# Kernel optimization log

Measured on AMD Instinct MI355X. Metric: run time of the kernel, lower is better.

The kernel has to match this reference:

```python
import jax, jax.numpy as jnp
import numpy as np

V, D, H, L, RATIO, T_MAX = 1024, 512, 8, 11, 3, 1024
DH = D // H
HID = D * RATIO
NB, DB = 2048, 128  # bigram buckets / dim
EPS = 1e-6


def _rope_tables(T):
    pos = jnp.arange(T, dtype=jnp.float32)
    freqs = 1.0 / (10000.0 ** (jnp.arange(0, DH, 2, dtype=jnp.float32) / DH))
    emb = jnp.outer(pos, freqs)  # [T, DH/2]
    return jnp.cos(emb), jnp.sin(emb)


def _rmsnorm(x, w):
    return x * jax.lax.rsqrt(jnp.mean(x * x, axis=-1, keepdims=True) + EPS) * w


def setup_inputs() -> dict:
    key = jax.random.key(0)
    ks = jax.random.split(key, 10)
    B, T = 8, 1024
    s = 0.02
    return {
        "x": jax.random.randint(ks[0], (B, T), 0, V),
        "embed": jax.random.normal(ks[1], (V, D), jnp.float32) * s,
        "Wqkv": jax.random.normal(ks[2], (L, 3 * D, D), jnp.float32) * s,
        "Wproj": jax.random.normal(ks[3], (L, D, D), jnp.float32) * s,
        "n1_w": jnp.ones((L, D), jnp.float32),
        "n2_w": jnp.ones((L, D), jnp.float32),
        "Wfc1": jax.random.normal(ks[4], (L, HID, D), jnp.float32) * s,
        "Wfc2": jax.random.normal(ks[5], (L, D, HID), jnp.float32) * s,
        "norm_f_w": jnp.ones((D,), jnp.float32),
        "bg_embed": jax.random.normal(ks[6], (NB, DB), jnp.float32) * s,
        "bg_proj": jax.random.normal(ks[7], (V, DB), jnp.float32) * s,
    }


def _attn(x, Wqkv, Wproj, cos, sin, causal):
    B, T, C = x.shape
    qkv = x @ Wqkv.T  # [B,T,3D]
    q, k, v = jnp.split(qkv, 3, axis=-1)
    def heads(t):
        return t.reshape(B, T, H, DH).transpose(0, 2, 1, 3)  # [B,H,T,DH]
    q, k, v = heads(q), heads(k), heads(v)
    c = cos[None, None]  # [1,1,T,DH/2]
    s = sin[None, None]
    def rope(t):
        t1, t2 = t[..., : DH // 2], t[..., DH // 2 :]
        return jnp.concatenate([t1 * c - t2 * s, t1 * s + t2 * c], axis=-1)
    q, k = rope(q), rope(k)
    w = jnp.einsum("bhqd,bhkd->bhqk", q, k) * (DH ** -0.5)
    w = jnp.where(causal, w, -jnp.inf)
    w = jax.nn.softmax(w.astype(jnp.float32), axis=-1).astype(x.dtype)
    out = jnp.einsum("bhqk,bhkd->bhqd", w, v)
    self_w = jnp.diagonal(w, axis1=-2, axis2=-1)[..., None]  # [B,H,T,1]
    out = out - self_w * v  # XSA: subtract self-value contribution
    out = out.transpose(0, 2, 1, 3).reshape(B, T, C)
    return out @ Wproj.T


def reference(x, embed, Wqkv, Wproj, n1_w, n2_w, Wfc1, Wfc2, norm_f_w, bg_embed, bg_proj):
    B, T = x.shape
    cos, sin = _rope_tables(T_MAX)
    cos, sin = cos[:T], sin[:T]
    causal = jnp.tril(jnp.ones((T, T), dtype=bool))
    # bigram logits from previous token
    prev = jnp.concatenate([jnp.zeros((B, 1), x.dtype), x[:, :-1]], axis=1)
    bigram_logits = bg_embed[prev % NB] @ bg_proj.T  # [B,T,V]
    h = embed[x]
    for i in range(L):
        h = h + _attn(_rmsnorm(h, n1_w[i]), Wqkv[i], Wproj[i], cos, sin, causal)
        z = _rmsnorm(h, n2_w[i])
        h = h + jnp.square(jax.nn.relu(z @ Wfc1[i].T)) @ Wfc2[i].T
    h = _rmsnorm(h, norm_f_w)
    return h @ embed.T + bigram_logits
```

## Files before the change

kernel.cpp:

```cpp
#include <hip/hip_runtime.h>

#define NROW   8192
#define DMODEL 512
#define TSEQ   1024
#define LAYERS 11
#define HIDDEN 1536

typedef __bf16 bf16_t;
typedef bf16_t bf16x8 __attribute__((ext_vector_type(8)));
typedef bf16_t bf16x4 __attribute__((ext_vector_type(4)));
typedef float  f32x4  __attribute__((ext_vector_type(4)));
typedef unsigned int u32;
typedef u32 u32x4 __attribute__((ext_vector_type(4)));

#define GLD16(gp, lp) __builtin_amdgcn_global_load_lds( \
    (const __attribute__((address_space(1))) void*)(gp), \
    (__attribute__((address_space(3))) void*)(lp), 16, 0, 0)

#if __has_builtin(__builtin_amdgcn_exp2f)
#define EXP2(x) __builtin_amdgcn_exp2f(x)
#else
#define EXP2(x) exp2f(x)
#endif

__global__ void rope_table_k(float* __restrict__ cosT, float* __restrict__ sinT) {
    int i = blockIdx.x * blockDim.x + threadIdx.x;
    int t = i >> 5, j = i & 31;
    float freq = powf(10000.f, -(float)j * (1.f / 32.f));
    float ang = (float)t * freq;
    cosT[i] = cosf(ang);
    sinT[i] = sinf(ang);
}

__global__ void embed_gather_k(const int* __restrict__ x,
                               const float* __restrict__ embed,
                               float* __restrict__ h,
                               bf16_t* __restrict__ hb) {
    int n = blockIdx.x;
    int d = threadIdx.x;
    float4 v = ((const float4*)(embed + (size_t)x[n] * DMODEL))[d];
    ((float4*)(h + (size_t)n * DMODEL))[d] = v;
    bf16x4 o;
    o[0] = (bf16_t)v.x; o[1] = (bf16_t)v.y; o[2] = (bf16_t)v.z; o[3] = (bf16_t)v.w;
    *(bf16x4*)(hb + (size_t)n * DMODEL + d * 4) = o;
}

__global__ void bg_gather_k(const int* __restrict__ x,
                            const float* __restrict__ bge,
                            bf16_t* __restrict__ Afu) {
    int n = blockIdx.x;
    int t = n & (TSEQ - 1);
    int prev = (t == 0) ? 0 : x[n - 1];
    Afu[(size_t)n * 640 + 512 + threadIdx.x] = (bf16_t)bge[(size_t)prev * 128 + threadIdx.x];
}

__global__ void cvt_bf16_k(const float* __restrict__ in, bf16_t* __restrict__ out, int n8) {
    int i = blockIdx.x * blockDim.x + threadIdx.x;
    if (i >= n8) return;
    float4 a = ((const float4*)in)[2 * i];
    float4 b = ((const float4*)in)[2 * i + 1];
    bf16x8 o;
    o[0] = (bf16_t)a.x; o[1] = (bf16_t)a.y; o[2] = (bf16_t)a.z; o[3] = (bf16_t)a.w;
    o[4] = (bf16_t)b.x; o[5] = (bf16_t)b.y; o[6] = (bf16_t)b.z; o[7] = (bf16_t)b.w;
    ((bf16x8*)out)[i] = o;
}

__global__ void cvt_fold_k(const float* __restrict__ in,
                           const float* __restrict__ nw,
                           bf16_t* __restrict__ out, int n8, int layerSz) {
    int i = blockIdx.x * blockDim.x + threadIdx.x;
    if (i >= n8) return;
    int i8 = i * 8;
    int k = i8 & 511;
    int l = i8 / layerSz;
    const float* wv = nw + l * DMODEL + k;
    float4 a = ((const float4*)in)[2 * i];
    float4 b = ((const float4*)in)[2 * i + 1];
    float4 wa = *(const float4*)wv;
    float4 wb = *(const float4*)(wv + 4);
    bf16x8 o;
    o[0] = (bf16_t)(a.x * wa.x); o[1] = (bf16_t)(a.y * wa.y);
    o[2] = (bf16_t)(a.z * wa.z); o[3] = (bf16_t)(a.w * wa.w);
    o[4] = (bf16_t)(b.x * wb.x); o[5] = (bf16_t)(b.y * wb.y);
    o[6] = (bf16_t)(b.z * wb.z); o[7] = (bf16_t)(b.w * wb.w);
    ((bf16x8*)out)[i] = o;
}

__global__ void cvt_pad_k(const float* __restrict__ in, bf16_t* __restrict__ out,
                          int n8, int lshift, int mask, int colOff) {
    int i = blockIdx.x * blockDim.x + threadIdx.x;
    if (i >= n8) return;
    int i8 = i * 8;
    int row = i8 >> lshift;
    int col = i8 & mask;
    float4 a = ((const float4*)in)[2 * i];
    float4 b = ((const float4*)in)[2 * i + 1];
    bf16x8 o;
    o[0] = (bf16_t)a.x; o[1] = (bf16_t)a.y; o[2] = (bf16_t)a.z; o[3] = (bf16_t)a.w;
    o[4] = (bf16_t)b.x; o[5] = (bf16_t)b.y; o[6] = (bf16_t)b.z; o[7] = (bf16_t)b.w;
    *(bf16x8*)&out[(size_t)row * 640 + colOff + col] = o;
}

__global__ __launch_bounds__(256) void scale_k(const bf16_t* __restrict__ hb,
                                               float* __restrict__ s) {
    int wv = threadIdx.x >> 6, lane = threadIdx.x & 63;
    int row = (blockIdx.x << 2) + wv;
    bf16x8 v = *(const bf16x8*)(hb + (size_t)row * DMODEL + lane * 8);
    float ss = 0.f;
#pragma unroll
    for (int j = 0; j < 8; ++j) { float f = (float)v[j]; ss += f * f; }
#pragma unroll
    for (int off = 32; off; off >>= 1) ss += __shfl_xor(ss, off, 64);
    if (lane == 0) s[row] = rsqrtf(ss * (1.f / DMODEL) + 1e-6f);
}

__global__ __launch_bounds__(256) void rmsnorm_k(const float* __restrict__ in,
                                                 const float* __restrict__ w,
                                                 bf16_t* __restrict__ out,
                                                 int ostride) {
    int wv = threadIdx.x >> 6, lane = threadIdx.x & 63;
    int row = (blockIdx.x << 2) + wv;
    const float* rp = in + (size_t)row * DMODEL + lane * 8;
    float4 v0 = *(const float4*)(rp);
    float4 v1 = *(const float4*)(rp + 4);
    float ss = v0.x*v0.x + v0.y*v0.y + v0.z*v0.z + v0.w*v0.w
             + v1.x*v1.x + v1.y*v1.y + v1.z*v1.z + v1.w*v1.w;
#pragma unroll
    for (int off = 32; off; off >>= 1) ss += __shfl_xor(ss, off, 64);
    float sc = rsqrtf(ss * (1.f / DMODEL) + 1e-6f);
    const float* wp = w + lane * 8;
    float4 w0 = *(const float4*)(wp);
    float4 w1 = *(const float4*)(wp + 4);
    bf16x8 o;
    o[0] = (bf16_t)(v0.x * sc * w0.x); o[1] = (bf16_t)(v0.y * sc * w0.y);
    o[2] = (bf16_t)(v0.z * sc * w0.z); o[3] = (bf16_t)(v0.w * sc * w0.w);
    o[4] = (bf16_t)(v1.x * sc * w1.x); o[5] = (bf16_t)(v1.y * sc * w1.y);
    o[6] = (bf16_t)(v1.z * sc * w1.z); o[7] = (bf16_t)(v1.w * sc * w1.w);
    *(bf16x8*)(out + (size_t)row * ostride + lane * 8) = o;
}

template<int BM, int EPI>
__global__ __launch_bounds__(256, 2)
void gemm_mfma(const bf16_t* __restrict__ A,
               const bf16_t* __restrict__ B,
               float* __restrict__ Cf,
               bf16_t* __restrict__ Cb,
               const float* __restrict__ cosT,
               const float* __restrict__ sinT,
               const float* __restrict__ Sc,
               int M, int N, int K, int nbx) {
    constexpr int NT  = 256;
    constexpr int WM  = 2;
    constexpr int MI  = BM / WM / 16;
    constexpr int ACH = (BM * 4) / NT;
    constexpr int BCH = 2;
    constexpr bool SCALED = (EPI == 2 || EPI == 4);
    __shared__ __align__(16) bf16_t As[3][BM * 32];
    __shared__ __align__(16) bf16_t Bs[3][128 * 32];
    const int tid = threadIdx.x;
    const int w = tid >> 6, lane = tid & 63;

    const int nwg = (int)gridDim.x;
    const int bid = blockIdx.x;
    const int swz = (bid & 7) * (nwg >> 3) + (bid >> 3);
    const int bx = swz % nbx, by = swz / nbx;

    const int m0 = by * BM, n0 = bx * 128;
    const int wr = (w >> 1) * (BM / WM), wc = (w & 1) * 64;
    const int fr = lane & 15, fq = lane >> 4;

    f32x4 acc[MI][4] = {};

    float sld[SCALED ? MI : 1][4];
    if constexpr (SCALED) {
#pragma unroll
        for (int i = 0; i < MI; ++i)
#pragma unroll
            for (int q = 0; q < 4; ++q)
                sld[i][q] = Sc[m0 + wr + i * 16 + fq * 4 + q];
    }
    float cold[EPI == 1 ? MI : 1][4][4];
    if constexpr (EPI == 1) {
#pragma unroll
        for (int i = 0; i < MI; ++i)
#pragma unroll
            for (int j = 0; j < 4; ++j)
#pragma unroll
                for (int q = 0; q < 4; ++q)
                    cold[i][j][q] = Cf[(size_t)(m0 + wr + i * 16 + fq * 4 + q) * N
                                       + n0 + wc + j * 16 + fr];
    }

    auto stage = [&](int k0, int buf) {
#pragma unroll
        for (int c = 0; c < ACH; ++c) {
            int idx = c * NT + tid;
            int row = idx >> 2, cs = idx & 3;
            GLD16(A + (size_t)(m0 + row) * K + k0 + cs * 8,
                  &As[buf][(size_t)(c * NT + w * 64) * 8]);
        }
#pragma unroll
        for (int c = 0; c < BCH; ++c) {
            int idx = c * NT + tid;
            int row = idx >> 2, cs = idx & 3;
            GLD16(B + (size_t)(n0 + row) * K + k0 + cs * 8,
                  &Bs[buf][(size_t)(c * NT + w * 64) * 8]);
        }
    };

    const int NK = K >> 5;
    stage(0, 0);
    stage(32, 1);
    for (int k = 0; k < NK; ++k) {
        const int cur = k % 3;
        if (k + 2 < NK) {
            stage((k + 2) << 5, (k + 2) % 3);
            if constexpr (BM == 128) asm volatile("s_waitcnt vmcnt(8)" ::: "memory");
            else                     asm volatile("s_waitcnt vmcnt(6)" ::: "memory");
        } else if (k + 1 < NK) {
            if constexpr (BM == 128) asm volatile("s_waitcnt vmcnt(4)" ::: "memory");
            else                     asm volatile("s_waitcnt vmcnt(3)" ::: "memory");
        } else {
            asm volatile("s_waitcnt vmcnt(0)" ::: "memory");
        }
        __builtin_amdgcn_s_barrier();
        __builtin_amdgcn_sched_barrier(0);

        bf16x8 a[MI], b[4];
        const bf16_t* ap = &As[cur][(size_t)(wr + fr) * 32 + fq * 8];
        const bf16_t* bp = &Bs[cur][(size_t)(wc + fr) * 32 + fq * 8];
#pragma unroll
        for (int i = 0; i < MI; ++i) a[i] = *(const bf16x8*)(ap + i * 16 * 32);
#pragma unroll
        for (int j = 0; j < 4; ++j)  b[j] = *(const bf16x8*)(bp + j * 16 * 32);
        __builtin_amdgcn_s_setprio(1);
#pragma unroll
        for (int i = 0; i < MI; ++i)
#pragma unroll
            for (int j = 0; j < 4; ++j)
                acc[i][j] = __builtin_amdgcn_mfma_f32_16x16x32_bf16(a[i], b[j], acc[i][j], 0, 0, 0);
        __builtin_amdgcn_s_setprio(0);

        asm volatile("s_waitcnt lgkmcnt(0)" ::: "memory");
        __builtin_amdgcn_s_barrier();
        __builtin_amdgcn_sched_barrier(0);
    }

    if (EPI == 4) {
        const bool qk = (n0 + wc) < 1024;
#pragma unroll
        for (int i = 0; i < MI; ++i) {
#pragma unroll
            for (int q = 0; q < 4; ++q) {
                int row = m0 + wr + i * 16 + fq * 4 + q;
                size_t rb = (size_t)row * N + n0 + wc;
                float sm = sld[i][q];
                if (qk) {
                    int t = row & (TSEQ - 1);
#pragma unroll
                    for (int j = 0; j < 2; ++j) {
                        int d = j * 16 + fr;
                        float c = cosT[t * 32 + d];
                        float s = sinT[t * 32 + d];
                        float v1 = acc[i][j][q] * sm, v2 = acc[i][j + 2][q] * sm;
                        Cb[rb + j * 16 + fr]       = (bf16_t)(v1 * c - v2 * s);
                        Cb[rb + (j + 2) * 16 + fr] = (bf16_t)(v1 * s + v2 * c);
                    }
                } else {
#pragma unroll
                    for (int j = 0; j < 4; ++j)
                        Cb[rb + j * 16 + fr] = (bf16_t)(acc[i][j][q] * sm);
                }
            }
        }
        return;
    }
#pragma unroll
    for (int i = 0; i < MI; ++i) {
        int row = m0 + wr + i * 16 + fq * 4;
#pragma unroll
        for (int j = 0; j < 4; ++j) {
            int col = n0 + wc + j * 16 + fr;
#pragma unroll
            for (int q = 0; q < 4; ++q) {
                float v = acc[i][j][q];
                size_t off = (size_t)(row + q) * N + col;
                if (EPI == 0)      Cf[off] = v;
                else if (EPI == 1) {
                    float nv = cold[i][j][q] + v;
                    Cf[off] = nv;
                    Cb[off] = (bf16_t)nv;
                } else if (EPI == 2) {
                    v = fmaxf(v * sld[i][q], 0.f);
                    Cb[off] = (bf16_t)(v * v);
                }
            }
        }
    }
}

__global__ __launch_bounds__(256) void attn_mfma_k(const bf16_t* __restrict__ qkvb,
                                                   bf16_t* __restrict__ outb) {
    __shared__ __align__(16) bf16_t Ks[2][64 * 64];
    __shared__ __align__(16) bf16_t VsT[2][2 * 64 * 32];

    const int tid = threadIdx.x;
    const int w  = tid >> 6;
    const int ln = tid & 63;
    const int lr = ln & 15;
    const int lg = ln >> 4;

    const int bid = blockIdx.x;
    const int qb = 15 - (bid >> 6);
    const int bh = bid & 63;
    const int b = bh >> 3, h = bh & 7;
    const int tq0b = qb << 6;
    const int tq0  = tq0b + w * 16;
    const int qrow = tq0 + lr;

    const bf16_t* Qg = qkvb + (size_t)b * TSEQ * 1536 + h * 64;
    const bf16_t* Kg = Qg + 512;
    const bf16_t* Vg = Qg + 1024;

    const int mk = tid >> 4;
    const int md = tid & 15;
    const int src0 = lr + 32 * (lg & 1);
    const int fsel = lg >> 1;
    const int gofs = 8 * (lg ^ ((lr >> 2) & 3));

    auto KSTAGE = [&](int t0, int buf) {
#pragma unroll
        for (int ii = 0; ii < 2; ++ii) {
            const int i = w * 2 + ii;
            int key = i * 8 + (ln >> 3);
            int dc  = (ln & 7) ^ (ln >> 3);
            GLD16(Kg + (size_t)(t0 + key) * 1536 + dc * 8, &Ks[buf][i * 512]);
        }
    };
    auto VLOAD = [&](int t0, bf16x4* rv) {
#pragma unroll
        for (int i = 0; i < 4; ++i)
            rv[i] = *(const bf16x4*)(Vg + (size_t)(t0 + mk * 4 + i) * 1536 + md * 4);
    };
    auto VWRITE = [&](const bf16x4* rv, int buf) {
        const int s = mk >> 3;
#pragma unroll
        for (int j = 0; j < 4; ++j) {
            int row = md * 4 + j;
            bf16x4 wv;
            wv[0] = rv[0][j]; wv[1] = rv[1][j]; wv[2] = rv[2][j]; wv[3] = rv[3][j];
            int g = (mk & 7) ^ ((md & 3) << 1);
            *(bf16x4*)&VsT[buf][s * 2048 + row * 32 + g * 4] = wv;
        }
    };

    bf16x8 qreg[2];
    {
        const float QS = 0.1803368801f;
        const bf16_t* qp = Qg + (size_t)qrow * 1536 + lg * 8;
        qreg[0] = *(const bf16x8*)qp;
        qreg[1] = *(const bf16x8*)(qp + 32);
#pragma unroll
        for (int j = 0; j < 8; ++j) {
            qreg[0][j] = (bf16_t)((float)qreg[0][j] * QS);
            qreg[1][j] = (bf16_t)((float)qreg[1][j] * QS);
        }
    }

    f32x4 accO[4] = {};
    float mrun = -1e30f, pl = 0.f, esf = 0.f;

    {
        bf16x4 rv[4];
        KSTAGE(0, 0);
        VLOAD(0, rv);
        asm volatile("s_waitcnt vmcnt(0)" ::: "memory");
        VWRITE(rv, 0);
        asm volatile("s_waitcnt lgkmcnt(0)" ::: "memory");
        __builtin_amdgcn_s_barrier();
        __builtin_amdgcn_sched_barrier(0);
    }

    for (int t0 = 0; t0 <= tq0b; t0 += 64) {
        const int cur = (t0 >> 6) & 1;
        const bool more = t0 < tq0b;
        const bool masked = t0 == tq0b;
        bf16x4 rv[4];
        if (more) {
            KSTAGE(t0 + 64, cur ^ 1);
            VLOAD(t0 + 64, rv);
        }

        f32x4 sq[4] = {};
        __builtin_amdgcn_s_setprio(1);
#pragma unroll
        for (int kr = 0; kr < 4; ++kr) {
            int key = kr * 16 + lr;
#pragma unroll
            for (int s = 0; s < 2; ++s) {
                int chunk = key * 8 + ((s * 4 + lg) ^ (key & 7));
                bf16x8 kf = *(const bf16x8*)&Ks[cur][chunk * 8];
                sq[kr] = __builtin_amdgcn_mfma_f32_16x16x32_bf16(kf, qreg[s], sq[kr], 0, 0, 0);
            }
        }
        __builtin_amdgcn_s_setprio(0);

        float e16[4][4];
        float tm = -1e30f;
        if (masked) {
#pragma unroll
            for (int f = 0; f < 4; ++f)
#pragma unroll
                for (int r = 0; r < 4; ++r) {
                    int key = t0 + f * 16 + lg * 4 + r;
                    float sv = (key <= qrow) ? sq[f][r] : -1e30f;
                    e16[f][r] = sv;
                    tm = fmaxf(tm, sv);
                }
        } else {
#pragma unroll
            for (int f = 0; f < 4; ++f)
#pragma unroll
                for (int r = 0; r < 4; ++r) {
                    e16[f][r] = sq[f][r];
                    tm = fmaxf(tm, sq[f][r]);
                }
        }
        tm = fmaxf(tm, __shfl_xor(tm, 16, 64));
        tm = fmaxf(tm, __shfl_xor(tm, 32, 64));

        const bool resc = __any(tm > mrun + 8.f);
        float mnew = resc ? fmaxf(mrun, tm) : mrun;
        float psum = 0.f;
#pragma unroll
        for (int f = 0; f < 4; ++f)
#pragma unroll
            for (int r = 0; r < 4; ++r) {
                float e = EXP2(e16[f][r] - mnew);
                e16[f][r] = e;
                psum += e;
            }
        float pd = 0.f;
        if (masked) {
#pragma unroll
            for (int f = 0; f < 4; ++f)
#pragma unroll
                for (int r = 0; r < 4; ++r) {
                    int key = t0 + f * 16 + lg * 4 + r;
                    pd = (key == qrow) ? e16[f][r] : pd;
                }
        }
        if (resc) {
            float corr = EXP2(mrun - mnew);
            mrun = mnew;
            pl  = pl  * corr + psum;
            esf = esf * corr + pd;
#pragma unroll
            for (int dblk = 0; dblk < 4; ++dblk)
#pragma unroll
                for (int r = 0; r < 4; ++r) accO[dblk][r] *= corr;
        } else {
            pl  += psum;
            esf += pd;
        }

        u32 plo[4], phi[4];
#pragma unroll
        for (int f = 0; f < 4; ++f) {
            bf16x4 t;
            t[0] = (bf16_t)e16[f][0]; t[1] = (bf16_t)e16[f][1];
            t[2] = (bf16_t)e16[f][2]; t[3] = (bf16_t)e16[f][3];
            uint2 pr = __builtin_bit_cast(uint2, t);
            plo[f] = pr.x; phi[f] = pr.y;
        }

#pragma unroll
        for (int s = 0; s < 2; ++s) {
            u32 a0 = (u32)__shfl((int)plo[s * 2],     src0,      64);
            u32 a1 = (u32)__shfl((int)phi[s * 2],     src0,      64);
            u32 a2 = (u32)__shfl((int)plo[s * 2],     src0 + 16, 64);
            u32 a3 = (u32)__shfl((int)phi[s * 2],     src0 + 16, 64);
            u32 c0 = (u32)__shfl((int)plo[s * 2 + 1], src0,      64);
            u32 c1 = (u32)__shfl((int)phi[s * 2 + 1], src0,      64);
            u32 c2 = (u32)__shfl((int)plo[s * 2 + 1], src0 + 16, 64);
            u32 c3 = (u32)__shfl((int)phi[s * 2 + 1], src0 + 16, 64);
            u32x4 bw;
            bw[0] = fsel ? c0 : a0;
            bw[1] = fsel ? c1 : a1;
            bw[2] = fsel ? c2 : a2;
            bw[3] = fsel ? c3 : a3;
            bf16x8 bfrag = __builtin_bit_cast(bf16x8, bw);
            __builtin_amdgcn_s_setprio(1);
#pragma unroll
            for (int dblk = 0; dblk < 4; ++dblk) {
                bf16x8 av = *(const bf16x8*)&VsT[cur][s * 2048 + (dblk * 16 + lr) * 32 + gofs];
                accO[dblk] = __builtin_amdgcn_mfma_f32_16x16x32_bf16(av, bfrag, accO[dblk], 0, 0, 0);
            }
            __builtin_amdgcn_s_setprio(0);
        }

        if (more) {
            asm volatile("s_waitcnt vmcnt(0)" ::: "memory");
            VWRITE(rv, cur ^ 1);
            asm volatile("s_waitcnt lgkmcnt(0)" ::: "memory");
            __builtin_amdgcn_s_barrier();
            __builtin_amdgcn_sched_barrier(0);
        }
    }

    pl  += __shfl_xor(pl, 16, 64);  pl  += __shfl_xor(pl, 32, 64);
    esf += __shfl_xor(esf, 16, 64); esf += __shfl_xor(esf, 32, 64);
    float rin = 1.0f / pl;
    const bf16_t* vqp = Vg + (size_t)qrow * 1536;
    bf16_t* op = outb + (size_t)(b * TSEQ + qrow) * DMODEL + h * 64;
#pragma unroll
    for (int dblk = 0; dblk < 4; ++dblk) {
        bf16x4 vq = *(const bf16x4*)(vqp + dblk * 16 + lg * 4);
        bf16x4 o4;
#pragma unroll
        for (int r = 0; r < 4; ++r)
            o4[r] = (bf16_t)((accO[dblk][r] - esf * (float)vq[r]) * rin);
        *(bf16x4*)(op + dblk * 16 + lg * 4) = o4;
    }
}

static inline void cvt(const float* in, bf16_t* out, size_t n, hipStream_t s) {
    int n8 = (int)(n / 8);
    cvt_bf16_k<<<(n8 + 255) / 256, 256, 0, s>>>(in, out, n8);
}

extern "C" void kernel_launch(void* const* d_in, const int* in_sizes, int n_in,
                              void* d_out, int out_size, void* d_ws, size_t ws_size,
                              hipStream_t stream) {
    const int*   x     = (const int*)d_in[0];
    const float* embed = (const float*)d_in[1];
    const float* Wqkv  = (const float*)d_in[2];
    const float* Wproj = (const float*)d_in[3];
    const float* n1w   = (const float*)d_in[4];
    const float* n2w   = (const float*)d_in[5];
    const float* Wfc1  = (const float*)d_in[6];
    const float* Wfc2  = (const float*)d_in[7];
    const float* normf = (const float*)d_in[8];
    const float* bge   = (const float*)d_in[9];
    const float* bgp   = (const float*)d_in[10];
    float* out = (float*)d_out;

    float* ws   = (float*)d_ws;
    float* cosT = ws;
    float* sinT = cosT + 32768;
    float* h    = sinT + 32768;
    bf16_t* qkvb = (bf16_t*)(h + (size_t)NROW * DMODEL);
    bf16_t* ub   = qkvb;
    bf16_t* Afu  = qkvb;
    bf16_t* hb   = qkvb + (size_t)NROW * 1536;
    bf16_t* atb  = hb  + (size_t)NROW * DMODEL;
    bf16_t* wqb  = atb + (size_t)NROW * DMODEL;
    bf16_t* wpb  = wqb + (size_t)LAYERS * 3 * DMODEL * DMODEL;
    bf16_t* w1b  = wpb + (size_t)LAYERS * DMODEL * DMODEL;
    bf16_t* w2b  = w1b + (size_t)LAYERS * HIDDEN * DMODEL;
    bf16_t* bfu  = w2b + (size_t)LAYERS * DMODEL * HIDDEN;
    float*  sbuf = (float*)(bfu + (size_t)1024 * 640);

    rope_table_k<<<128, 256, 0, stream>>>(cosT, sinT);
    embed_gather_k<<<NROW, 128, 0, stream>>>(x, embed, h, hb);

    {
        int n8q = (int)((size_t)LAYERS * 3 * DMODEL * DMODEL / 8);
        cvt_fold_k<<<(n8q + 255) / 256, 256, 0, stream>>>(Wqkv, n1w, wqb, n8q, 3 * DMODEL * DMODEL);
        int n81 = (int)((size_t)LAYERS * HIDDEN * DMODEL / 8);
        cvt_fold_k<<<(n81 + 255) / 256, 256, 0, stream>>>(Wfc1, n2w, w1b, n81, HIDDEN * DMODEL);
    }
    cvt(Wproj, wpb, (size_t)LAYERS * DMODEL * DMODEL, stream);
    cvt(Wfc2,  w2b, (size_t)LAYERS * DMODEL * HIDDEN, stream);
    cvt_pad_k<<<(65536 + 255) / 256, 256, 0, stream>>>(embed, bfu, 65536, 9, 511, 0);
    cvt_pad_k<<<(16384 + 255) / 256, 256, 0, stream>>>(bgp,   bfu, 16384, 7, 127, 512);

    for (int i = 0; i < LAYERS; ++i) {
        scale_k<<<NROW / 4, 256, 0, stream>>>(hb, sbuf);
        gemm_mfma<128, 4><<<768, 256, 0, stream>>>(
            hb, wqb + (size_t)i * 3 * DMODEL * DMODEL, nullptr, qkvb,
            cosT, sinT, sbuf, NROW, 3 * DMODEL, DMODEL, 12);
        attn_mfma_k<<<1024, 256, 0, stream>>>(qkvb, atb);
        gemm_mfma<64, 1><<<512, 256, 0, stream>>>(
            atb, wpb + (size_t)i * DMODEL * DMODEL, h, hb,
            nullptr, nullptr, nullptr, NROW, DMODEL, DMODEL, 4);
        scale_k<<<NROW / 4, 256, 0, stream>>>(hb, sbuf);
        gemm_mfma<128, 2><<<768, 256, 0, stream>>>(
            hb, w1b + (size_t)i * HIDDEN * DMODEL, nullptr, ub,
            nullptr, nullptr, sbuf, NROW, HIDDEN, DMODEL, 12);
        gemm_mfma<64, 1><<<512, 256, 0, stream>>>(
            ub, w2b + (size_t)i * DMODEL * HIDDEN, h, hb,
            nullptr, nullptr, nullptr, NROW, DMODEL, HIDDEN, 4);
    }

    rmsnorm_k<<<NROW / 4, 256, 0, stream>>>(h, normf, Afu, 640);
    bg_gather_k<<<NROW, 128, 0, stream>>>(x, bge, Afu);
    gemm_mfma<128, 0><<<512, 256, 0, stream>>>(
        Afu, bfu, out, nullptr, nullptr, nullptr, nullptr, NROW, 1024, 640, 8);
}
```

Measured before the change: 1.499 ms.

## Share K/V tiles across 128-query attention blocks and deepen GEMM ring buffer

The attention kernel now launches 512 blocks of 512 threads. Each block covers 128 query rows, so every K/V tile loaded into shared memory serves twice as many query waves, which halves the K/V global loads per output. Waves in the lower 64-row half skip compute on the final key tile but still reach the barriers. Separately, the BM=64 GEMM gets a 4-deep LDS ring, which makes the end-of-iteration barrier and lgkmcnt wait unnecessary. The cost is more LDS use per block and some wave idling on the diagonal tile.

Result: faster. 1.444 ms (-3.7%).

```diff
diff --git a/kernel.cpp b/kernel.cpp
--- a/kernel.cpp
+++ b/kernel.cpp
@@ -154,9 +154,10 @@
     constexpr int MI  = BM / WM / 16;
     constexpr int ACH = (BM * 4) / NT;
     constexpr int BCH = 2;
+    constexpr int NBUF = (BM == 64) ? 4 : 3;
     constexpr bool SCALED = (EPI == 2 || EPI == 4);
-    __shared__ __align__(16) bf16_t As[3][BM * 32];
-    __shared__ __align__(16) bf16_t Bs[3][128 * 32];
+    __shared__ __align__(16) bf16_t As[NBUF][BM * 32];
+    __shared__ __align__(16) bf16_t Bs[NBUF][128 * 32];
     const int tid = threadIdx.x;
     const int w = tid >> 6, lane = tid & 63;
 
@@ -212,9 +213,9 @@
     stage(0, 0);
     stage(32, 1);
     for (int k = 0; k < NK; ++k) {
-        const int cur = k % 3;
+        const int cur = k % NBUF;
         if (k + 2 < NK) {
-            stage((k + 2) << 5, (k + 2) % 3);
+            stage((k + 2) << 5, (k + 2) % NBUF);
             if constexpr (BM == 128) asm volatile("s_waitcnt vmcnt(8)" ::: "memory");
             else                     asm volatile("s_waitcnt vmcnt(6)" ::: "memory");
         } else if (k + 1 < NK) {
@@ -241,9 +242,11 @@
                 acc[i][j] = __builtin_amdgcn_mfma_f32_16x16x32_bf16(a[i], b[j], acc[i][j], 0, 0, 0);
         __builtin_amdgcn_s_setprio(0);
 
-        asm volatile("s_waitcnt lgkmcnt(0)" ::: "memory");
-        __builtin_amdgcn_s_barrier();
-        __builtin_amdgcn_sched_barrier(0);
+        if constexpr (NBUF == 3) {
+            asm volatile("s_waitcnt lgkmcnt(0)" ::: "memory");
+            __builtin_amdgcn_s_barrier();
+            __builtin_amdgcn_sched_barrier(0);
+        }
     }
 
     if (EPI == 4) {
@@ -299,7 +302,7 @@
     }
 }
 
-__global__ __launch_bounds__(256) void attn_mfma_k(const bf16_t* __restrict__ qkvb,
+__global__ __launch_bounds__(512) void attn_mfma_k(const bf16_t* __restrict__ qkvb,
                                                    bf16_t* __restrict__ outb) {
     __shared__ __align__(16) bf16_t Ks[2][64 * 64];
     __shared__ __align__(16) bf16_t VsT[2][2 * 64 * 32];
@@ -311,12 +314,13 @@
     const int lg = ln >> 4;
 
     const int bid = blockIdx.x;
-    const int qb = 15 - (bid >> 6);
+    const int p  = 7 - (bid >> 6);
     const int bh = bid & 63;
     const int b = bh >> 3, h = bh & 7;
-    const int tq0b = qb << 6;
-    const int tq0  = tq0b + w * 16;
+    const int lastT = (p << 7) + 64;
+    const int tq0  = (p << 7) + w * 16;
     const int qrow = tq0 + lr;
+    const int wlast = tq0 & ~63;
 
     const bf16_t* Qg = qkvb + (size_t)b * TSEQ * 1536 + h * 64;
     const bf16_t* Kg = Qg + 512;
@@ -329,13 +333,9 @@
     const int gofs = 8 * (lg ^ ((lr >> 2) & 3));
 
     auto KSTAGE = [&](int t0, int buf) {
-#pragma unroll
-        for (int ii = 0; ii < 2; ++ii) {
-            const int i = w * 2 + ii;
-            int key = i * 8 + (ln >> 3);
-            int dc  = (ln & 7) ^ (ln >> 3);
-            GLD16(Kg + (size_t)(t0 + key) * 1536 + dc * 8, &Ks[buf][i * 512]);
-        }
+        int key = w * 8 + (ln >> 3);
+        int dc  = (ln & 7) ^ (ln >> 3);
+        GLD16(Kg + (size_t)(t0 + key) * 1536 + dc * 8, &Ks[buf][w * 512]);
     };
     auto VLOAD = [&](int t0, bf16x4* rv) {
 #pragma unroll
@@ -373,135 +373,138 @@
     {
         bf16x4 rv[4];
         KSTAGE(0, 0);
-        VLOAD(0, rv);
+        if (w < 4) VLOAD(0, rv);
         asm volatile("s_waitcnt vmcnt(0)" ::: "memory");
-        VWRITE(rv, 0);
+        if (w < 4) VWRITE(rv, 0);
         asm volatile("s_waitcnt lgkmcnt(0)" ::: "memory");
         __builtin_amdgcn_s_barrier();
         __builtin_amdgcn_sched_barrier(0);
     }
 
-    for (int t0 = 0; t0 <= tq0b; t0 += 64) {
+    for (int t0 = 0; t0 <= lastT; t0 += 64) {
         const int cur = (t0 >> 6) & 1;
-        const bool more = t0 < tq0b;
-        const bool masked = t0 == tq0b;
+        const bool more = t0 < lastT;
         bf16x4 rv[4];
         if (more) {
             KSTAGE(t0 + 64, cur ^ 1);
-            VLOAD(t0 + 64, rv);
-        }
-
-        f32x4 sq[4] = {};
-        __builtin_amdgcn_s_setprio(1);
-#pragma unroll
-        for (int kr = 0; kr < 4; ++kr) {
-            int key = kr * 16 + lr;
+            if (w < 4) VLOAD(t0 + 64, rv);
+        }
+
+        if (t0 <= wlast) {
+            const bool masked = t0 == wlast;
+
+            f32x4 sq[4] = {};
+            __builtin_amdgcn_s_setprio(1);
+#pragma unroll
+            for (int kr = 0; kr < 4; ++kr) {
+                int key = kr * 16 + lr;
+#pragma unroll
+                for (int s = 0; s < 2; ++s) {
+                    int chunk = key * 8 + ((s * 4 + lg) ^ (key & 7));
+                    bf16x8 kf = *(const bf16x8*)&Ks[cur][chunk * 8];
+                    sq[kr] = __builtin_amdgcn_mfma_f32_16x16x32_bf16(kf, qreg[s], sq[kr], 0, 0, 0);
+                }
+            }
+            __builtin_amdgcn_s_setprio(0);
+
+            float e16[4][4];
+            float tm = -1e30f;
+            if (masked) {
+#pragma unroll
+                for (int f = 0; f < 4; ++f)
+#pragma unroll
+                    for (int r = 0; r < 4; ++r) {
+                        int key = t0 + f * 16 + lg * 4 + r;
+                        float sv = (key <= qrow) ? sq[f][r] : -1e30f;
+                        e16[f][r] = sv;
+                        tm = fmaxf(tm, sv);
+                    }
+            } else {
+#pragma unroll
+                for (int f = 0; f < 4; ++f)
+#pragma unroll
+                    for (int r = 0; r < 4; ++r) {
+                        e16[f][r] = sq[f][r];
+                        tm = fmaxf(tm, sq[f][r]);
+                    }
+            }
+            tm = fmaxf(tm, __shfl_xor(tm, 16, 64));
+            tm = fmaxf(tm, __shfl_xor(tm, 32, 64));
+
+            const bool resc = __any(tm > mrun + 8.f);
+            float mnew = resc ? fmaxf(mrun, tm) : mrun;
+            float psum = 0.f;
+#pragma unroll
+            for (int f = 0; f < 4; ++f)
+#pragma unroll
+                for (int r = 0; r < 4; ++r) {
+                    float e = EXP2(e16[f][r] - mnew);
+                    e16[f][r] = e;
+                    psum += e;
+                }
+            float pd = 0.f;
+            if (masked) {
+#pragma unroll
+                for (int f = 0; f < 4; ++f)
+#pragma unroll
+                    for (int r = 0; r < 4; ++r) {
+                        int key = t0 + f * 16 + lg * 4 + r;
+                        pd = (key == qrow) ? e16[f][r] : pd;
+                    }
+            }
+            if (resc) {
+                float corr = EXP2(mrun - mnew);
+                mrun = mnew;
+                pl  = pl  * corr + psum;
+                esf = esf * corr + pd;
+#pragma unroll
+                for (int dblk = 0; dblk < 4; ++dblk)
+#pragma unroll
+                    for (int r = 0; r < 4; ++r) accO[dblk][r] *= corr;
+            } else {
+                pl  += psum;
+                esf += pd;
+            }
+
+            u32 plo[4], phi[4];
+#pragma unroll
+            for (int f = 0; f < 4; ++f) {
+                bf16x4 t;
+                t[0] = (bf16_t)e16[f][0]; t[1] = (bf16_t)e16[f][1];
+                t[2] = (bf16_t)e16[f][2]; t[3] = (bf16_t)e16[f][3];
+                uint2 pr = __builtin_bit_cast(uint2, t);
+                plo[f] = pr.x; phi[f] = pr.y;
+            }
+
 #pragma unroll
             for (int s = 0; s < 2; ++s) {
-                int chunk = key * 8 + ((s * 4 + lg) ^ (key & 7));
-                bf16x8 kf = *(const bf16x8*)&Ks[cur][chunk * 8];
-                sq[kr] = __builtin_amdgcn_mfma_f32_16x16x32_bf16(kf, qreg[s], sq[kr], 0, 0, 0);
-            }
-        }
-        __builtin_amdgcn_s_setprio(0);
-
-        float e16[4][4];
-        float tm = -1e30f;
-        if (masked) {
-#pragma unroll
-            for (int f = 0; f < 4; ++f)
-#pragma unroll
-                for (int r = 0; r < 4; ++r) {
-                    int key = t0 + f * 16 + lg * 4 + r;
-                    float sv = (key <= qrow) ? sq[f][r] : -1e30f;
-                    e16[f][r] = sv;
-                    tm = fmaxf(tm, sv);
+                u32 a0 = (u32)__shfl((int)plo[s * 2],     src0,      64);
+                u32 a1 = (u32)__shfl((int)phi[s * 2],     src0,      64);
+                u32 a2 = (u32)__shfl((int)plo[s * 2],     src0 + 16, 64);
+                u32 a3 = (u32)__shfl((int)phi[s * 2],     src0 + 16, 64);
+                u32 c0 = (u32)__shfl((int)plo[s * 2 + 1], src0,      64);
+                u32 c1 = (u32)__shfl((int)phi[s * 2 + 1], src0,      64);
+                u32 c2 = (u32)__shfl((int)plo[s * 2 + 1], src0 + 16, 64);
+                u32 c3 = (u32)__shfl((int)phi[s * 2 + 1], src0 + 16, 64);
+                u32x4 bw;
+                bw[0] = fsel ? c0 : a0;
+                bw[1] = fsel ? c1 : a1;
+                bw[2] = fsel ? c2 : a2;
+                bw[3] = fsel ? c3 : a3;
+                bf16x8 bfrag = __builtin_bit_cast(bf16x8, bw);
+                __builtin_amdgcn_s_setprio(1);
+#pragma unroll
+                for (int dblk = 0; dblk < 4; ++dblk) {
+                    bf16x8 av = *(const bf16x8*)&VsT[cur][s * 2048 + (dblk * 16 + lr) * 32 + gofs];
+                    accO[dblk] = __builtin_amdgcn_mfma_f32_16x16x32_bf16(av, bfrag, accO[dblk], 0, 0, 0);
                 }
-        } else {
-#pragma unroll
-            for (int f = 0; f < 4; ++f)
-#pragma unroll
-                for (int r = 0; r < 4; ++r) {
-                    e16[f][r] = sq[f][r];
-                    tm = fmaxf(tm, sq[f][r]);
-                }
-        }
-        tm = fmaxf(tm, __shfl_xor(tm, 16, 64));
-        tm = fmaxf(tm, __shfl_xor(tm, 32, 64));
-
-        const bool resc = __any(tm > mrun + 8.f);
-        float mnew = resc ? fmaxf(mrun, tm) : mrun;
-        float psum = 0.f;
-#pragma unroll
-        for (int f = 0; f < 4; ++f)
-#pragma unroll
-            for (int r = 0; r < 4; ++r) {
-                float e = EXP2(e16[f][r] - mnew);
-                e16[f][r] = e;
-                psum += e;
-            }
-        float pd = 0.f;
-        if (masked) {
-#pragma unroll
-            for (int f = 0; f < 4; ++f)
-#pragma unroll
-                for (int r = 0; r < 4; ++r) {
-                    int key = t0 + f * 16 + lg * 4 + r;
-                    pd = (key == qrow) ? e16[f][r] : pd;
-                }
-        }
-        if (resc) {
-            float corr = EXP2(mrun - mnew);
-            mrun = mnew;
-            pl  = pl  * corr + psum;
-            esf = esf * corr + pd;
-#pragma unroll
-            for (int dblk = 0; dblk < 4; ++dblk)
-#pragma unroll
-                for (int r = 0; r < 4; ++r) accO[dblk][r] *= corr;
-        } else {
-            pl  += psum;
-            esf += pd;
-        }
-
-        u32 plo[4], phi[4];
-#pragma unroll
-        for (int f = 0; f < 4; ++f) {
-            bf16x4 t;
-            t[0] = (bf16_t)e16[f][0]; t[1] = (bf16_t)e16[f][1];
-            t[2] = (bf16_t)e16[f][2]; t[3] = (bf16_t)e16[f][3];
-            uint2 pr = __builtin_bit_cast(uint2, t);
-            plo[f] = pr.x; phi[f] = pr.y;
-        }
-
-#pragma unroll
-        for (int s = 0; s < 2; ++s) {
-            u32 a0 = (u32)__shfl((int)plo[s * 2],     src0,      64);
-            u32 a1 = (u32)__shfl((int)phi[s * 2],     src0,      64);
-            u32 a2 = (u32)__shfl((int)plo[s * 2],     src0 + 16, 64);
-            u32 a3 = (u32)__shfl((int)phi[s * 2],     src0 + 16, 64);
-            u32 c0 = (u32)__shfl((int)plo[s * 2 + 1], src0,      64);
-            u32 c1 = (u32)__shfl((int)phi[s * 2 + 1], src0,      64);
-            u32 c2 = (u32)__shfl((int)plo[s * 2 + 1], src0 + 16, 64);
-            u32 c3 = (u32)__shfl((int)phi[s * 2 + 1], src0 + 16, 64);
-            u32x4 bw;
-            bw[0] = fsel ? c0 : a0;
-            bw[1] = fsel ? c1 : a1;
-            bw[2] = fsel ? c2 : a2;
-            bw[3] = fsel ? c3 : a3;
-            bf16x8 bfrag = __builtin_bit_cast(bf16x8, bw);
-            __builtin_amdgcn_s_setprio(1);
-#pragma unroll
-            for (int dblk = 0; dblk < 4; ++dblk) {
-                bf16x8 av = *(const bf16x8*)&VsT[cur][s * 2048 + (dblk * 16 + lr) * 32 + gofs];
-                accO[dblk] = __builtin_amdgcn_mfma_f32_16x16x32_bf16(av, bfrag, accO[dblk], 0, 0, 0);
-            }
-            __builtin_amdgcn_s_setprio(0);
+                __builtin_amdgcn_s_setprio(0);
+            }
         }
 
         if (more) {
             asm volatile("s_waitcnt vmcnt(0)" ::: "memory");
-            VWRITE(rv, cur ^ 1);
+            if (w < 4) VWRITE(rv, cur ^ 1);
             asm volatile("s_waitcnt lgkmcnt(0)" ::: "memory");
             __builtin_amdgcn_s_barrier();
             __builtin_amdgcn_sched_barrier(0);
@@ -580,7 +583,7 @@
         gemm_mfma<128, 4><<<768, 256, 0, stream>>>(
             hb, wqb + (size_t)i * 3 * DMODEL * DMODEL, nullptr, qkvb,
             cosT, sinT, sbuf, NROW, 3 * DMODEL, DMODEL, 12);
-        attn_mfma_k<<<1024, 256, 0, stream>>>(qkvb, atb);
+        attn_mfma_k<<<512, 512, 0, stream>>>(qkvb, atb);
         gemm_mfma<64, 1><<<512, 256, 0, stream>>>(
             atb, wpb + (size_t)i * DMODEL * DMODEL, h, hb,
             nullptr, nullptr, nullptr, NROW, DMODEL, DMODEL, 4);
```
